# Performance work log

Measured on AMD Instinct MI355X. Metric: run time of the kernel, lower is better.

Reference implementation:

```python
import jax, jax.numpy as jnp
import numpy as np

SEQ, D, H = 4096, 1024, 16
HD = D // H
SCALE = HD ** -0.5


def setup_inputs() -> dict:
    key = jax.random.key(0)
    ks = jax.random.split(key, 8)
    s = 0.02
    return {
        "hidden_states": jax.random.normal(ks[0], (SEQ, D), dtype=jnp.float32),
        "wq": jax.random.normal(ks[1], (D, D), dtype=jnp.float32) * s,
        "bq": jax.random.normal(ks[2], (D,), dtype=jnp.float32) * s,
        "wk": jax.random.normal(ks[3], (D, D), dtype=jnp.float32) * s,
        "wv": jax.random.normal(ks[4], (D, D), dtype=jnp.float32) * s,
        "bv": jax.random.normal(ks[5], (D,), dtype=jnp.float32) * s,
        "wo": jax.random.normal(ks[6], (D, D), dtype=jnp.float32) * s,
        "bo": jax.random.normal(ks[7], (D,), dtype=jnp.float32) * s,
    }


def reference(hidden_states, wq, bq, wk, wv, bv, wo, bo):
    S = hidden_states.shape[0]
    # torch Linear: y = x @ W^T + b  (k_proj has no bias)
    q = (hidden_states @ wq.T + bq).reshape(S, H, HD).transpose(1, 0, 2)  # [H,S,hd]
    k = (hidden_states @ wk.T).reshape(S, H, HD).transpose(1, 0, 2)       # [H,S,hd]
    v = (hidden_states @ wv.T + bv).reshape(S, H, HD).transpose(1, 0, 2)  # [H,S,hd]
    scores = jnp.einsum('hqd,hkd->hqk', q, k) * SCALE                     # [H,S,S]
    # softmax computed in fp32 then cast back to query dtype
    attn = jax.nn.softmax(scores.astype(jnp.float32), axis=-1).astype(q.dtype)
    out = jnp.einsum('hqk,hkd->hqd', attn, v)                             # [H,S,hd]
    out = out.transpose(1, 0, 2).reshape(S, D)
    return out @ wo.T + bo
```

## Files before the change

### kernel.cpp

```cpp
#include <hip/hip_runtime.h>

#define SEQ 4096
#define DIM 1024
#define NH 16
#define HD 64
#define QKVSTR 3072

typedef __attribute__((ext_vector_type(8))) short bf16x8;
typedef __attribute__((ext_vector_type(4))) float f32x4;
typedef __attribute__((ext_vector_type(16))) float f32x16;
typedef __attribute__((ext_vector_type(4))) unsigned int uint4v;

__device__ __forceinline__ unsigned short f2bf(float f) {
  unsigned int b = __float_as_uint(f);
  b = b + 0x7fffu + ((b >> 16) & 1u);
  return (unsigned short)(b >> 16);
}

__device__ __forceinline__ unsigned int cvt_pk_bf16(float lo, float hi) {
  unsigned int r;
  asm("v_cvt_pk_bf16_f32 %0, %1, %2" : "=v"(r) : "v"(lo), "v"(hi));
  return r;
}

__device__ __forceinline__ float fast_exp2(float x) {
#if __has_builtin(__builtin_amdgcn_exp2f)
  return __builtin_amdgcn_exp2f(x);
#else
  float r; asm("v_exp_f32 %0, %1" : "=v"(r) : "v"(x)); return r;
#endif
}

typedef __attribute__((address_space(3))) unsigned int lds_uint;
typedef __attribute__((address_space(1))) const unsigned int global_uint;

__device__ __forceinline__ void gload_lds16(const void* g, void* l) {
  __builtin_amdgcn_global_load_lds((global_uint*)g, (lds_uint*)l, 16, 0, 0);
}

__global__ __launch_bounds__(256) void cast_bf16_kernel(
    const float* __restrict__ in, unsigned short* __restrict__ out, int n8, float scale) {
  int i = blockIdx.x * blockDim.x + threadIdx.x;
  if (i >= n8) return;
  const float4* p = (const float4*)in + (size_t)i * 2;
  float4 x0 = p[0], x1 = p[1];
  union { unsigned short u[8]; uint4v v; } o;
  o.u[0] = f2bf(x0.x * scale); o.u[1] = f2bf(x0.y * scale);
  o.u[2] = f2bf(x0.z * scale); o.u[3] = f2bf(x0.w * scale);
  o.u[4] = f2bf(x1.x * scale); o.u[5] = f2bf(x1.y * scale);
  o.u[6] = f2bf(x1.z * scale); o.u[7] = f2bf(x1.w * scale);
  *((uint4v*)out + i) = o.v;
}

template<int BIASMODE, int OUT_F32>
__global__ __launch_bounds__(256) void gemm_bt_kernel(
    const unsigned short* __restrict__ A, const unsigned short* __restrict__ B,
    const float* __restrict__ b0, const float* __restrict__ b1, float qscale,
    void* __restrict__ Cout, int M, int N, int K) {
  __shared__ unsigned short As[128 * 32];
  __shared__ unsigned short Bs[128 * 32];
  int tid = threadIdx.x;
  int wave = tid >> 6, lane = tid & 63;
  int g = lane >> 4, lc = lane & 15;
  int wm = wave >> 1, wn = wave & 1;
  int m0 = blockIdx.y * 128, n0 = blockIdx.x * 128;

  f32x4 acc[4][4] = {};

  for (int k0 = 0; k0 < K; k0 += 32) {
    __syncthreads();
    for (int c = 0; c < 2; ++c) {
      int chunk = c * 256 + wave * 64 + lane;
      int row = chunk >> 2, cb = chunk & 3;
      gload_lds16(A + (size_t)(m0 + row) * K + k0 + cb * 8, As + (c * 256 + wave * 64) * 8);
      gload_lds16(B + (size_t)(n0 + row) * K + k0 + cb * 8, Bs + (c * 256 + wave * 64) * 8);
    }
    __syncthreads();
    bf16x8 af[4], bfr[4];
    for (int mf = 0; mf < 4; ++mf)
      af[mf] = *(const bf16x8*)&As[(wm * 64 + mf * 16 + lc) * 32 + g * 8];
    for (int nf = 0; nf < 4; ++nf)
      bfr[nf] = *(const bf16x8*)&Bs[(wn * 64 + nf * 16 + lc) * 32 + g * 8];
    for (int mf = 0; mf < 4; ++mf)
      for (int nf = 0; nf < 4; ++nf)
        acc[mf][nf] = __builtin_amdgcn_mfma_f32_16x16x32_bf16(af[mf], bfr[nf], acc[mf][nf], 0, 0, 0);
  }

  for (int nf = 0; nf < 4; ++nf) {
    int col = n0 + wn * 64 + nf * 16 + lc;
    float bias = 0.f;
    if (BIASMODE == 1) {
      int sect = col >> 10, cc = col & 1023;
      bias = (sect == 0) ? b0[cc] * qscale : ((sect == 2) ? b1[cc] : 0.f);
    } else if (BIASMODE == 2) {
      bias = b0[col];
    }
    for (int mf = 0; mf < 4; ++mf) {
      int row = m0 + wm * 64 + mf * 16 + g * 4;
      for (int r = 0; r < 4; ++r) {
        float v = acc[mf][nf][r] + bias;
        if (OUT_F32) ((float*)Cout)[(size_t)(row + r) * N + col] = v;
        else ((unsigned short*)Cout)[(size_t)(row + r) * N + col] = f2bf(v);
      }
    }
  }
}

__global__ __launch_bounds__(256) void transpose_kernel(
    const unsigned short* __restrict__ V, unsigned short* __restrict__ Vt) {
  __shared__ unsigned short Ts[64 * 72];
  int tid = threadIdx.x;
  int s0 = blockIdx.x * 64, d0 = blockIdx.y * 64;
  for (int c = 0; c < 2; ++c) {
    int q = c * 256 + tid;
    int r = q >> 3, cb = q & 7;
    uint4v v = *(const uint4v*)&V[(size_t)(s0 + r) * QKVSTR + d0 + cb * 8];
    *(uint4v*)&Ts[r * 72 + cb * 8] = v;
  }
  __syncthreads();
  for (int c = 0; c < 2; ++c) {
    int q = c * 256 + tid;
    int d = q >> 3, sc = q & 7;
    union { unsigned short u[8]; uint4v v; } ov;
    for (int j = 0; j < 8; ++j) ov.u[j] = Ts[(sc * 8 + j) * 72 + d];
    *(uint4v*)&Vt[(size_t)(d0 + d) * SEQ + s0 + sc * 8] = ov.v;
  }
}

__global__ __launch_bounds__(256) void attn_kernel(
    const unsigned short* __restrict__ QKV, const unsigned short* __restrict__ Vt,
    unsigned short* __restrict__ Aout) {
  __shared__ unsigned short Qs[128 * 64];
  __shared__ unsigned short Ks[2][64 * 64];
  __shared__ unsigned short Vs[2][64 * 64];
  int tid = threadIdx.x;
  int w = tid >> 6, lane = tid & 63;
  int hi = lane >> 5, l31 = lane & 31;
  int h = blockIdx.y;
  int q0 = blockIdx.x * 128;
  const unsigned short* Qg = QKV + h * HD;
  const unsigned short* Kg = QKV + DIM + h * HD;
  const unsigned short* Vg = Vt + (size_t)(h * HD) * SEQ;

  for (int c = 0; c < 4; ++c) {
    int chunk = c * 256 + w * 64 + lane;
    int row = chunk >> 3, pos = chunk & 7;
    int db = pos ^ (row & 7);
    gload_lds16(Qg + (size_t)(q0 + row) * QKVSTR + db * 8, Qs + (c * 256 + w * 64) * 8);
  }

  auto stage_kv = [&](int buf, int kv0) {
    for (int c = 0; c < 2; ++c) {
      int chunk = c * 256 + w * 64 + lane;
      int row = chunk >> 3, pos = chunk & 7;
      int db = pos ^ (row & 7);
      gload_lds16(Kg + (size_t)(kv0 + row) * QKVSTR + db * 8, &Ks[buf][(c * 256 + w * 64) * 8]);
      gload_lds16(Vg + (size_t)row * SEQ + kv0 + db * 8, &Vs[buf][(c * 256 + w * 64) * 8]);
    }
  };
  stage_kv(0, 0);
  __syncthreads();

  bf16x8 qf[4];
  {
    int qrow = w * 32 + l31;
    for (int dc = 0; dc < 4; ++dc) {
      int pos = 2 * dc + hi;
      qf[dc] = *(const bf16x8*)&Qs[qrow * 64 + (pos ^ (qrow & 7)) * 8];
    }
  }

  f32x16 o0 = {}, o1 = {};
  float lsum = 0.f;
  int cur = 0;

  for (int t = 0; t < SEQ / 64; ++t) {
    if (t + 1 < SEQ / 64) stage_kv(cur ^ 1, (t + 1) * 64);

    bf16x8 kf[2][4];
    for (int f = 0; f < 2; ++f)
      for (int dc = 0; dc < 4; ++dc) {
        int krow = f * 32 + l31;
        int pos = 2 * dc + hi;
        kf[f][dc] = *(const bf16x8*)&Ks[cur][krow * 64 + (pos ^ (krow & 7)) * 8];
      }
    f32x16 st0 = {}, st1 = {};
    for (int dc = 0; dc < 4; ++dc) {
      st0 = __builtin_amdgcn_mfma_f32_32x32x16_bf16(kf[0][dc], qf[dc], st0, 0, 0, 0);
      st1 = __builtin_amdgcn_mfma_f32_32x32x16_bf16(kf[1][dc], qf[dc], st1, 0, 0, 0);
    }

    float p0[16], p1[16];
    float ls = 0.f;
#pragma unroll
    for (int r = 0; r < 16; ++r) { p0[r] = fast_exp2(st0[r]); ls += p0[r]; }
#pragma unroll
    for (int r = 0; r < 16; ++r) { p1[r] = fast_exp2(st1[r]); ls += p1[r]; }
    lsum += ls;

    bf16x8 pa[4];
#pragma unroll
    for (int f = 0; f < 2; ++f) {
      const float* pp = f ? p1 : p0;
#pragma unroll
      for (int cc = 0; cc < 2; ++cc) {
        unsigned uLO0 = cvt_pk_bf16(pp[8 * cc + 0], pp[8 * cc + 1]);
        unsigned uLO1 = cvt_pk_bf16(pp[8 * cc + 2], pp[8 * cc + 3]);
        unsigned uHI0 = cvt_pk_bf16(pp[8 * cc + 4], pp[8 * cc + 5]);
        unsigned uHI1 = cvt_pk_bf16(pp[8 * cc + 6], pp[8 * cc + 7]);
        auto s0 = __builtin_amdgcn_permlane32_swap(uLO0, uHI0, false, false);
        auto s1 = __builtin_amdgcn_permlane32_swap(uLO1, uHI1, false, false);
        union { unsigned u[4]; bf16x8 v; } pw;
        pw.u[0] = s0[0]; pw.u[1] = s1[0]; pw.u[2] = s0[1]; pw.u[3] = s1[1];
        pa[f * 2 + cc] = pw.v;
      }
    }

#pragma unroll
    for (int c = 0; c < 4; ++c) {
      int pos = 2 * c + hi;
      int r0 = l31, r1 = 32 + l31;
      bf16x8 vf0 = *(const bf16x8*)&Vs[cur][r0 * 64 + (pos ^ (r0 & 7)) * 8];
      bf16x8 vf1 = *(const bf16x8*)&Vs[cur][r1 * 64 + (pos ^ (r1 & 7)) * 8];
      o0 = __builtin_amdgcn_mfma_f32_32x32x16_bf16(pa[c], vf0, o0, 0, 0, 0);
      o1 = __builtin_amdgcn_mfma_f32_32x32x16_bf16(pa[c], vf1, o1, 0, 0, 0);
    }

    __syncthreads();
    cur ^= 1;
  }

  lsum += __shfl_xor(lsum, 32);
  float inv = 1.f / lsum;
#pragma unroll
  for (int r = 0; r < 16; ++r) {
    int qr = (r & 3) + 8 * (r >> 2) + 4 * hi;
    float ir = __shfl(inv, qr + (lane & 32));
    size_t row = q0 + w * 32 + qr;
    Aout[row * DIM + h * HD + l31]      = f2bf(o0[r] * ir);
    Aout[row * DIM + h * HD + 32 + l31] = f2bf(o1[r] * ir);
  }
}

extern "C" void kernel_launch(void* const* d_in, const int* in_sizes, int n_in,
                              void* d_out, int out_size, void* d_ws, size_t ws_size,
                              hipStream_t stream) {
  (void)in_sizes; (void)n_in; (void)out_size; (void)ws_size;
  const float* X  = (const float*)d_in[0];
  const float* wq = (const float*)d_in[1];
  const float* bq = (const float*)d_in[2];
  const float* wk = (const float*)d_in[3];
  const float* wv = (const float*)d_in[4];
  const float* bv = (const float*)d_in[5];
  const float* wo = (const float*)d_in[6];
  const float* bo = (const float*)d_in[7];

  char* ws = (char*)d_ws;
  const size_t SZ_XD  = (size_t)SEQ * DIM * 2;
  const size_t SZ_W   = (size_t)DIM * DIM * 2;
  const size_t SZ_QKV = (size_t)SEQ * QKVSTR * 2;
  unsigned short* Xb   = (unsigned short*)(ws);
  unsigned short* Wqkv = (unsigned short*)(ws + SZ_XD);
  unsigned short* Wob  = (unsigned short*)(ws + SZ_XD + 3 * SZ_W);
  unsigned short* QKVb = (unsigned short*)(ws + SZ_XD + 4 * SZ_W);
  unsigned short* Vtb  = (unsigned short*)(ws + SZ_XD + 4 * SZ_W + SZ_QKV);
  unsigned short* Ab   = Xb;

  const float QSCALE = 0.125f * 1.44269504088896f;
  int nX8 = SEQ * DIM / 8, nW8 = DIM * DIM / 8;
  cast_bf16_kernel<<<nX8 / 256, 256, 0, stream>>>(X,  Xb, nX8, 1.f);
  cast_bf16_kernel<<<nW8 / 256, 256, 0, stream>>>(wq, Wqkv,                nW8, QSCALE);
  cast_bf16_kernel<<<nW8 / 256, 256, 0, stream>>>(wk, Wqkv + (size_t)DIM * DIM,     nW8, 1.f);
  cast_bf16_kernel<<<nW8 / 256, 256, 0, stream>>>(wv, Wqkv + (size_t)2 * DIM * DIM, nW8, 1.f);
  cast_bf16_kernel<<<nW8 / 256, 256, 0, stream>>>(wo, Wob, nW8, 1.f);

  gemm_bt_kernel<1, 0><<<dim3(QKVSTR / 128, SEQ / 128), 256, 0, stream>>>(
      Xb, Wqkv, bq, bv, QSCALE, QKVb, SEQ, QKVSTR, DIM);

  transpose_kernel<<<dim3(SEQ / 64, DIM / 64), 256, 0, stream>>>(QKVb + 2 * DIM, Vtb);

  attn_kernel<<<dim3(SEQ / 128, NH), 256, 0, stream>>>(QKVb, Vtb, Ab);

  gemm_bt_kernel<2, 1><<<dim3(DIM / 128, SEQ / 128), 256, 0, stream>>>(
      Ab, Wob, bo, nullptr, 1.f, d_out, SEQ, DIM, DIM);
}
```

Baseline: 177.5 us.

## Pipeline attention KV loads with partial vmcnt waits, setprio, and XCD block swizzle

Reworks the attention main loop so the next KV tile's global-to-LDS loads are issued unconditionally (wrapping on the last iteration) and only partially waited with vmcnt(4), replacing full __syncthreads with raw s_barrier plus sched_barrier fences. V fragments are hoisted ahead of the softmax so LDS reads overlap exp work, and MFMA sections are wrapped in s_setprio to favour matrix issue. The grid is flattened and block ids are swizzled so blocks sharing a head land on the same XCD for L2 reuse. In exchange the final iteration issues a redundant load, and correctness now depends on the hand-written wait counts and barrier placement.

```diff
diff --git a/kernel.cpp b/kernel.cpp
--- a/kernel.cpp
+++ b/kernel.cpp
@@ -136,11 +136,28 @@
   int tid = threadIdx.x;
   int w = tid >> 6, lane = tid & 63;
   int hi = lane >> 5, l31 = lane & 31;
-  int h = blockIdx.y;
-  int q0 = blockIdx.x * 128;
+
+  int bid = blockIdx.x;
+  int swz = (bid & 7) * 64 + (bid >> 3);
+  int h = swz >> 5;
+  int q0 = (swz & 31) * 128;
+
   const unsigned short* Qg = QKV + h * HD;
   const unsigned short* Kg = QKV + DIM + h * HD;
   const unsigned short* Vg = Vt + (size_t)(h * HD) * SEQ;
+
+  int ch0 = w * 64 + lane;
+  int r0s = ch0 >> 3, d0s = (ch0 & 7) ^ (r0s & 7);
+  int ch1 = 256 + ch0;
+  int r1s = ch1 >> 3, d1s = (ch1 & 7) ^ (r1s & 7);
+  int koff0 = r0s * QKVSTR + d0s * 8;
+  int koff1 = r1s * QKVSTR + d1s * 8;
+  int voff0 = r0s * SEQ + d0s * 8;
+  int voff1 = r1s * SEQ + d1s * 8;
+  unsigned short* ldsK_lo[2] = { &Ks[0][(w * 64) * 8],       &Ks[1][(w * 64) * 8] };
+  unsigned short* ldsK_hi[2] = { &Ks[0][(256 + w * 64) * 8], &Ks[1][(256 + w * 64) * 8] };
+  unsigned short* ldsV_lo[2] = { &Vs[0][(w * 64) * 8],       &Vs[1][(w * 64) * 8] };
+  unsigned short* ldsV_hi[2] = { &Vs[0][(256 + w * 64) * 8], &Vs[1][(256 + w * 64) * 8] };
 
   for (int c = 0; c < 4; ++c) {
     int chunk = c * 256 + w * 64 + lane;
@@ -148,18 +165,17 @@
     int db = pos ^ (row & 7);
     gload_lds16(Qg + (size_t)(q0 + row) * QKVSTR + db * 8, Qs + (c * 256 + w * 64) * 8);
   }
-
-  auto stage_kv = [&](int buf, int kv0) {
-    for (int c = 0; c < 2; ++c) {
-      int chunk = c * 256 + w * 64 + lane;
-      int row = chunk >> 3, pos = chunk & 7;
-      int db = pos ^ (row & 7);
-      gload_lds16(Kg + (size_t)(kv0 + row) * QKVSTR + db * 8, &Ks[buf][(c * 256 + w * 64) * 8]);
-      gload_lds16(Vg + (size_t)row * SEQ + kv0 + db * 8, &Vs[buf][(c * 256 + w * 64) * 8]);
-    }
-  };
-  stage_kv(0, 0);
-  __syncthreads();
+  {
+    const unsigned short* Kt = Kg;
+    const unsigned short* Vtt = Vg;
+    gload_lds16(Kt + koff0, ldsK_lo[0]);
+    gload_lds16(Kt + koff1, ldsK_hi[0]);
+    gload_lds16(Vtt + voff0, ldsV_lo[0]);
+    gload_lds16(Vtt + voff1, ldsV_hi[0]);
+  }
+  asm volatile("s_waitcnt vmcnt(4)" ::: "memory");
+  __builtin_amdgcn_sched_barrier(0);
+  __builtin_amdgcn_s_barrier();
 
   bf16x8 qf[4];
   {
@@ -175,7 +191,20 @@
   int cur = 0;
 
   for (int t = 0; t < SEQ / 64; ++t) {
-    if (t + 1 < SEQ / 64) stage_kv(cur ^ 1, (t + 1) * 64);
+    {
+      int kvn = ((t + 1) & (SEQ / 64 - 1)) * 64;
+      const unsigned short* Kt = Kg + (size_t)kvn * QKVSTR;
+      const unsigned short* Vtt = Vg + kvn;
+      int nb = cur ^ 1;
+      gload_lds16(Kt + koff0, ldsK_lo[nb]);
+      gload_lds16(Kt + koff1, ldsK_hi[nb]);
+      gload_lds16(Vtt + voff0, ldsV_lo[nb]);
+      gload_lds16(Vtt + voff1, ldsV_hi[nb]);
+    }
+    asm volatile("s_waitcnt vmcnt(4)" ::: "memory");
+    __builtin_amdgcn_sched_barrier(0);
+    __builtin_amdgcn_s_barrier();
+    __builtin_amdgcn_sched_barrier(0);
 
     bf16x8 kf[2][4];
     for (int f = 0; f < 2; ++f)
@@ -185,9 +214,20 @@
         kf[f][dc] = *(const bf16x8*)&Ks[cur][krow * 64 + (pos ^ (krow & 7)) * 8];
       }
     f32x16 st0 = {}, st1 = {};
+    __builtin_amdgcn_s_setprio(1);
     for (int dc = 0; dc < 4; ++dc) {
       st0 = __builtin_amdgcn_mfma_f32_32x32x16_bf16(kf[0][dc], qf[dc], st0, 0, 0, 0);
       st1 = __builtin_amdgcn_mfma_f32_32x32x16_bf16(kf[1][dc], qf[dc], st1, 0, 0, 0);
+    }
+    __builtin_amdgcn_s_setprio(0);
+
+    bf16x8 vf0[4], vf1[4];
+#pragma unroll
+    for (int c = 0; c < 4; ++c) {
+      int pos = 2 * c + hi;
+      int r0 = l31, r1 = 32 + l31;
+      vf0[c] = *(const bf16x8*)&Vs[cur][r0 * 64 + (pos ^ (r0 & 7)) * 8];
+      vf1[c] = *(const bf16x8*)&Vs[cur][r1 * 64 + (pos ^ (r1 & 7)) * 8];
     }
 
     float p0[16], p1[16];
@@ -216,17 +256,17 @@
       }
     }
 
+    __builtin_amdgcn_s_setprio(1);
 #pragma unroll
     for (int c = 0; c < 4; ++c) {
-      int pos = 2 * c + hi;
-      int r0 = l31, r1 = 32 + l31;
-      bf16x8 vf0 = *(const bf16x8*)&Vs[cur][r0 * 64 + (pos ^ (r0 & 7)) * 8];
-      bf16x8 vf1 = *(const bf16x8*)&Vs[cur][r1 * 64 + (pos ^ (r1 & 7)) * 8];
-      o0 = __builtin_amdgcn_mfma_f32_32x32x16_bf16(pa[c], vf0, o0, 0, 0, 0);
-      o1 = __builtin_amdgcn_mfma_f32_32x32x16_bf16(pa[c], vf1, o1, 0, 0, 0);
-    }
-
-    __syncthreads();
+      o0 = __builtin_amdgcn_mfma_f32_32x32x16_bf16(pa[c], vf0[c], o0, 0, 0, 0);
+      o1 = __builtin_amdgcn_mfma_f32_32x32x16_bf16(pa[c], vf1[c], o1, 0, 0, 0);
+    }
+    __builtin_amdgcn_s_setprio(0);
+
+    asm volatile("" ::: "memory");
+    __builtin_amdgcn_sched_barrier(0);
+    __builtin_amdgcn_s_barrier();
     cur ^= 1;
   }
 
@@ -279,7 +319,7 @@
 
   transpose_kernel<<<dim3(SEQ / 64, DIM / 64), 256, 0, stream>>>(QKVb + 2 * DIM, Vtb);
 
-  attn_kernel<<<dim3(SEQ / 128, NH), 256, 0, stream>>>(QKVb, Vtb, Ab);
+  attn_kernel<<<SEQ / 128 * NH, 256, 0, stream>>>(QKVb, Vtb, Ab);
 
   gemm_bt_kernel<2, 1><<<dim3(DIM / 128, SEQ / 128), 256, 0, stream>>>(
       Ab, Wob, bo, nullptr, 1.f, d_out, SEQ, DIM, DIM);
```

Measured after the change: 179.2 us. About the same (+1.0%).
